# Performance work log

Measured on AMD Instinct MI355X. Metric: run time of the kernel, lower is better.

Reference implementation:

```python
import jax, jax.numpy as jnp
import numpy as np

B, S, HID, H = 8, 1024, 2048, 16
D = HID // H  # head dim 128
MAX_LEN, SCALE_BASE, THETA_BASE, EPS = 1024, 512.0, 10000.0, 1e-5


def setup_inputs() -> dict:
    key = jax.random.key(0)
    ks = jax.random.split(key, 10)
    std = 0.02
    n_layers_scale = std / np.sqrt(24.0)
    return {
        "activations": jax.random.normal(ks[0], (B, S, HID), jnp.float32),
        "cache_k": jnp.zeros((B, MAX_LEN, H, D), jnp.float32),
        "cache_v": jnp.zeros((B, MAX_LEN, H, D), jnp.float32),
        "index": 0,
        "ln1_w": jnp.ones((HID,), jnp.float32),
        "ln2_w": jnp.ones((HID,), jnp.float32),
        "q_w": std * jax.random.normal(ks[1], (HID, HID), jnp.float32),
        "k_w": std * jax.random.normal(ks[2], (HID, HID), jnp.float32),
        "v_w": std * jax.random.normal(ks[3], (HID, HID), jnp.float32),
        "o_w": n_layers_scale * jax.random.normal(ks[4], (HID, HID), jnp.float32),
        "w1": std * jax.random.normal(ks[5], (4 * HID, HID), jnp.float32),
        "w2": n_layers_scale * jax.random.normal(ks[6], (HID, 4 * HID), jnp.float32),
    }


def _ln(x, w):
    m = jnp.mean(x, axis=-1, keepdims=True)
    v = jnp.mean((x - m) ** 2, axis=-1, keepdims=True)
    return (x - m) * jax.lax.rsqrt(v + EPS) * w


def _rotate_every_two(x):
    return jnp.stack((-x[..., 1::2], x[..., 0::2]), axis=-1).reshape(x.shape)


def _xpos_consts(start, end):
    drange = jnp.arange(2, D + 2, 2, dtype=jnp.float32)
    theta = jnp.repeat((1.0 / THETA_BASE) ** (drange / D), 2)
    alpha = 0.4 * D
    zeta = jnp.repeat((drange / (D / 2) + alpha) / (1 + alpha), 2)
    half = MAX_LEN // 2
    seq = (jnp.arange(-half, MAX_LEN - half, dtype=jnp.float32) / SCALE_BASE)[start:end]
    seq = seq[:, None, None]  # [S,1,1]
    c = jnp.cos(seq * theta[None, None, :])  # [S,1,D]
    s = jnp.sin(seq * theta[None, None, :])
    t = zeta[None, None, :] ** seq
    return c, s, t


def reference(activations, cache_k, cache_v, index, ln1_w, ln2_w, q_w, k_w, v_w, o_w, w1, w2):
    xn = _ln(activations, ln1_w)
    q = (xn @ q_w.T).reshape(B, S, H, D)
    k = (xn @ k_w.T).reshape(B, S, H, D)
    v = (xn @ v_w.T).reshape(B, S, H, D)
    # NOTE: source applies xpos to (keys, values), exactly as written
    c, s, t = _xpos_consts(index, index + S)
    k = (k * c + _rotate_every_two(k) * s) * t
    v = (v * c + _rotate_every_two(v) * s) / t
    # index==0 and S==MAX_LEN -> get_full_kv returns incoming kv, mask None (causal)
    scale = 1.0 / np.sqrt(D)
    scores = jnp.einsum("bqhd,bkhd->bhqk", q, k) * scale
    causal = jnp.tril(jnp.ones((S, S), bool))
    scores = jnp.where(causal[None, None], scores, -jnp.inf)
    attn = jax.nn.softmax(scores, axis=-1)
    ctx = jnp.einsum("bhqk,bkhd->bqhd", attn, v).reshape(B, S, HID)
    acts = activations + ctx @ o_w.T
    h = jax.nn.gelu(_ln(acts, ln2_w) @ w1.T, approximate=False)
    acts = acts + h @ w2.T
    return acts, cache_k, cache_v
```

## Files before the change

### kernel.cpp

```cpp
#include <hip/hip_runtime.h>
#include <hip/hip_bf16.h>
#include <math.h>

#define B_ 8
#define S_ 1024
#define HID_ 2048
#define H_ 16
#define D_ 128

typedef __attribute__((ext_vector_type(8))) short bf16x8;
typedef __attribute__((ext_vector_type(4))) float f32x4;

__device__ inline unsigned short f2b_raw(float f){
  union { __hip_bfloat16 h; unsigned short u; } cv; cv.h = __float2bfloat16(f); return cv.u;
}

__device__ inline void async_copy16(const void* g, void* l){
  __builtin_amdgcn_global_load_lds((const __attribute__((address_space(1))) unsigned int*)g,
                                   (__attribute__((address_space(3))) unsigned int*)l, 16, 0, 0);
}

__global__ __launch_bounds__(256) void cvt_all(const float* __restrict__ qw, const float* __restrict__ kw,
                                               const float* __restrict__ vw, const float* __restrict__ ow,
                                               const float* __restrict__ w1, const float* __restrict__ w2,
                                               unsigned short* __restrict__ dst){
  int i = blockIdx.x*256 + threadIdx.x;
  if (i >= 12582912) return;
  const float* src;
  int local;
  if      (i <  1048576){ src = qw; local = i; }
  else if (i <  2097152){ src = kw; local = i - 1048576; }
  else if (i <  3145728){ src = vw; local = i - 2097152; }
  else if (i <  4194304){ src = ow; local = i - 3145728; }
  else if (i <  8388608){ src = w1; local = i - 4194304; }
  else                  { src = w2; local = i - 8388608; }
  float4 f = ((const float4*)src)[local];
  ushort4 o;
  o.x = f2b_raw(f.x); o.y = f2b_raw(f.y); o.z = f2b_raw(f.z); o.w = f2b_raw(f.w);
  ((ushort4*)dst)[i] = o;
}

__global__ __launch_bounds__(256) void ln_kernel(const float* __restrict__ x,
                                                 const float* __restrict__ w,
                                                 unsigned short* __restrict__ y){
  const int row = blockIdx.x, tid = threadIdx.x;
  const float* xr = x + (size_t)row*HID_;
  float4 a = ((const float4*)xr)[tid];
  float4 b = ((const float4*)xr)[tid+256];
  float s  = a.x+a.y+a.z+a.w + b.x+b.y+b.z+b.w;
  float ss = a.x*a.x+a.y*a.y+a.z*a.z+a.w*a.w + b.x*b.x+b.y*b.y+b.z*b.z+b.w*b.w;
  #pragma unroll
  for (int off=1; off<64; off<<=1){ s += __shfl_xor(s, off, 64); ss += __shfl_xor(ss, off, 64); }
  __shared__ float red[8];
  int wv = tid>>6;
  if ((tid&63)==0){ red[wv]=s; red[4+wv]=ss; }
  __syncthreads();
  s  = red[0]+red[1]+red[2]+red[3];
  ss = red[4]+red[5]+red[6]+red[7];
  float mean = s * (1.0f/HID_);
  float var  = ss * (1.0f/HID_) - mean*mean;
  float rstd = rsqrtf(var + 1e-5f);
  float4 w0 = ((const float4*)w)[tid];
  float4 w1v = ((const float4*)w)[tid+256];
  ushort4 o0, o1;
  o0.x = f2b_raw((a.x-mean)*rstd*w0.x); o0.y = f2b_raw((a.y-mean)*rstd*w0.y);
  o0.z = f2b_raw((a.z-mean)*rstd*w0.z); o0.w = f2b_raw((a.w-mean)*rstd*w0.w);
  o1.x = f2b_raw((b.x-mean)*rstd*w1v.x); o1.y = f2b_raw((b.y-mean)*rstd*w1v.y);
  o1.z = f2b_raw((b.z-mean)*rstd*w1v.z); o1.w = f2b_raw((b.w-mean)*rstd*w1v.w);
  *(ushort4*)(y + (size_t)row*HID_ + tid*4) = o0;
  *(ushort4*)(y + (size_t)row*HID_ + 1024 + tid*4) = o1;
}

template<int EPI, int TAG>
__global__ __launch_bounds__(256) void gemm_bt(
    const unsigned short* __restrict__ A, const unsigned short* __restrict__ W,
    unsigned short* __restrict__ out_b, float* __restrict__ out_f,
    const float* __restrict__ res,
    unsigned short* __restrict__ k_out, unsigned short* __restrict__ vt_out,
    const int* __restrict__ idxp,
    int M, int N, int K, float scale)
{
  __shared__ unsigned short smem[16384];
  unsigned short* sA = smem;
  unsigned short* sB = smem + 8192;
  const int tid = threadIdx.x;
  const int lane = tid & 63, wv = tid >> 6;
  const int wm = wv >> 1, wn = wv & 1;
  const int lm = lane & 15, lg = lane >> 4;
  const int m0 = blockIdx.y * 128, n0 = blockIdx.x * 128;

  f32x4 acc[4][4];
  #pragma unroll
  for (int r=0;r<4;r++)
    #pragma unroll
    for (int c=0;c<4;c++) acc[r][c] = (f32x4){0.f,0.f,0.f,0.f};

  int offA[4][2], offB[4][2];
  #pragma unroll
  for (int r=0;r<4;r++)
    #pragma unroll
    for (int kc=0;kc<2;kc++){
      int rowA = wm*64 + r*16 + lm;
      int rowB = wn*64 + r*16 + lm;
      offA[r][kc] = rowA*64 + (((kc*4+lg) ^ (lm&7))*8);
      offB[r][kc] = rowB*64 + (((kc*4+lg) ^ (lm&7))*8);
    }

  for (int kk=0; kk<K; kk+=64){
    #pragma unroll
    for (int i=0;i<4;i++){
      int unit = i*256 + tid;
      int row = unit >> 3, us = unit & 7;
      int ku = us ^ (row & 7);
      int ldsoff = (unit & ~63) * 8;
      async_copy16(A + (size_t)(m0+row)*K + kk + ku*8, sA + ldsoff);
      async_copy16(W + (size_t)(n0+row)*K + kk + ku*8, sB + ldsoff);
    }
    __syncthreads();
    #pragma unroll
    for (int kc=0;kc<2;kc++){
      bf16x8 af[4], bfr[4];
      #pragma unroll
      for (int r=0;r<4;r++) af[r]  = *(const bf16x8*)(sA + offA[r][kc]);
      #pragma unroll
      for (int c=0;c<4;c++) bfr[c] = *(const bf16x8*)(sB + offB[c][kc]);
      #pragma unroll
      for (int r=0;r<4;r++)
        #pragma unroll
        for (int c=0;c<4;c++)
          acc[r][c] = __builtin_amdgcn_mfma_f32_16x16x32_bf16(af[r], bfr[c], acc[r][c], 0,0,0);
    }
    __syncthreads();
  }

  if (EPI == 0){
    const int region = n0 >> 11;
    const int idx0 = idxp[0];
    const int b  = m0 >> 10;
    const int s0g = m0 & 1023;
    const int hh = (n0 & 2047) >> 7;
    #pragma unroll
    for (int r=0;r<4;r++){
      #pragma unroll
      for (int c=0;c<4;c++){
        const int row0 = m0 + wm*64 + r*16 + lg*4;
        const int col  = n0 + wn*64 + c*16 + lm;
        const int d = col & 127;
        const int s0 = row0 & 1023;
        if (region == 0){
          #pragma unroll
          for (int g=0; g<4; g++)
            out_b[(((size_t)b*H_ + hh)*S_ + s0 + g)*D_ + d] = f2b_raw(acc[r][c][g]*scale);
        } else {
          const float fp = (float)((d>>1) + 1);
          const float theta = exp2f(fp * -0.2076205059304601f);
          const float zeta  = (fp*0.03125f + 51.2f) * (1.0f/52.2f);
          const float lz = log2f(zeta);
          const float sgn = (d & 1) ? 1.0f : -1.0f;
          #pragma unroll
          for (int g=0; g<4; g++){
            float va = acc[r][c][g];
            float part = __shfl_xor(va, 1, 64);
            float seq = ((float)(idx0 + s0 + g) - 512.0f) * (1.0f/512.0f);
            float ang = seq * theta;
            float sn, cc;
            __sincosf(ang, &sn, &cc);
            float rot = va*cc + sgn*part*sn;
            if (region == 1){
              float t = exp2f(seq * lz);
              k_out[(((size_t)b*H_ + hh)*S_ + s0 + g)*D_ + d] = f2b_raw(rot * t);
            } else {
              float ti = exp2f(-seq * lz);
              int d_local = wn*64 + c*16 + lm;
              int s_local = wm*64 + r*16 + lg*4 + g;
              int s8 = s_local >> 3;
              smem[d_local*128 + ((s8 ^ (d_local & 7))*8) + (s_local & 7)] = f2b_raw(rot * ti);
            }
          }
        }
      }
    }
    if (region == 2){
      __syncthreads();
      #pragma unroll
      for (int i=0;i<8;i++){
        int f = i*256 + tid;
        int dl = f >> 4, u = f & 15;
        int us = u ^ (dl & 7);
        uint4 val = *(const uint4*)(smem + dl*128 + us*8);
        *(uint4*)(vt_out + ((size_t)((size_t)b*H_ + hh)*D_ + dl)*S_ + s0g + u*8) = val;
      }
    }
  } else {
    #pragma unroll
    for (int r=0;r<4;r++){
      #pragma unroll
      for (int c=0;c<4;c++){
        int row0 = m0 + wm*64 + r*16 + lg*4;
        int col  = n0 + wn*64 + c*16 + lm;
        #pragma unroll
        for (int g=0; g<4; g++){
          int rr = row0 + g;
          float vacc = acc[r][c][g];
          if (EPI == 1){
            size_t o = (size_t)rr*N + col;
            out_f[o] = vacc + res[o];
          } else {
            size_t o = (size_t)rr*N + col;
            out_b[o] = f2b_raw(0.5f*vacc*(1.0f + erff(vacc*0.70710678118654752f)));
          }
        }
      }
    }
  }
}

__global__ __launch_bounds__(256) void flash_attn(
    const unsigned short* __restrict__ Q, const unsigned short* __restrict__ Kx,
    const unsigned short* __restrict__ VT, unsigned short* __restrict__ ctx)
{
  __shared__ unsigned short sK[64*136];
  __shared__ unsigned short sVT[128*72];
  __shared__ unsigned short sP[4][16*72];
  const int tid = threadIdx.x, lane = tid & 63, wv = tid >> 6;
  const int lm = lane & 15, lg = lane >> 4;
  const int qt = blockIdx.x, bh = blockIdx.y;
  const size_t base = (size_t)bh * S_ * D_;
  const int qr = qt*64 + wv*16;

  bf16x8 aq[4];
  #pragma unroll
  for (int kc=0;kc<4;kc++)
    aq[kc] = *(const bf16x8*)(Q + base + (size_t)(qr + lm)*D_ + kc*32 + lg*8);

  f32x4 accO[8];
  #pragma unroll
  for (int n=0;n<8;n++) accO[n] = (f32x4){0.f,0.f,0.f,0.f};
  float mrow[4] = {-INFINITY,-INFINITY,-INFINITY,-INFINITY};
  float lrow[4] = {0.f,0.f,0.f,0.f};
  unsigned short* myP = &sP[wv][0];

  for (int kt=0; kt<=qt; ++kt){
    int k0 = kt*64;
    __syncthreads();
    #pragma unroll
    for (int i=0;i<4;i++){
      int chunk = i*256 + tid;
      int krow = chunk >> 4, c8 = chunk & 15;
      *(uint4*)(sK + krow*136 + c8*8) = *(const uint4*)(Kx + base + (size_t)(k0+krow)*D_ + c8*8);
      int dd = chunk >> 3, c4 = chunk & 7;
      *(uint4*)(sVT + dd*72 + c4*8) = *(const uint4*)(VT + base + (size_t)dd*S_ + k0 + c4*8);
    }
    __syncthreads();
    f32x4 sc[4];
    #pragma unroll
    for (int n=0;n<4;n++){
      sc[n] = (f32x4){0.f,0.f,0.f,0.f};
      #pragma unroll
      for (int kc=0;kc<4;kc++){
        bf16x8 bk = *(const bf16x8*)(sK + (n*16+lm)*136 + kc*32 + lg*8);
        sc[n] = __builtin_amdgcn_mfma_f32_16x16x32_bf16(aq[kc], bk, sc[n], 0,0,0);
      }
    }
    if (kt == qt){
      #pragma unroll
      for (int n=0;n<4;n++)
        #pragma unroll
        for (int g=0; g<4; g++)
          if (k0 + n*16 + lm > qr + lg*4 + g) sc[n][g] = -INFINITY;
    }
    float mnew[4], alpha[4];
    #pragma unroll
    for (int g=0; g<4; g++){
      float mx = fmaxf(fmaxf(sc[0][g], sc[1][g]), fmaxf(sc[2][g], sc[3][g]));
      #pragma unroll
      for (int off=1; off<16; off<<=1) mx = fmaxf(mx, __shfl_xor(mx, off, 16));
      mnew[g] = fmaxf(mrow[g], mx);
      alpha[g] = __expf(mrow[g] - mnew[g]);
      mrow[g] = mnew[g];
    }
    #pragma unroll
    for (int n=0;n<4;n++)
      #pragma unroll
      for (int g=0; g<4; g++)
        sc[n][g] = __expf(sc[n][g] - mnew[g]);
    #pragma unroll
    for (int g=0; g<4; g++){
      float sum = sc[0][g]+sc[1][g]+sc[2][g]+sc[3][g];
      #pragma unroll
      for (int off=1; off<16; off<<=1) sum += __shfl_xor(sum, off, 16);
      lrow[g] = lrow[g]*alpha[g] + sum;
    }
    #pragma unroll
    for (int n=0;n<8;n++)
      #pragma unroll
      for (int g=0; g<4; g++) accO[n][g] *= alpha[g];
    #pragma unroll
    for (int n=0;n<4;n++)
      #pragma unroll
      for (int g=0; g<4; g++)
        myP[(lg*4+g)*72 + n*16 + lm] = f2b_raw(sc[n][g]);
    #pragma unroll
    for (int kc=0;kc<2;kc++){
      bf16x8 ap = *(const bf16x8*)(myP + lm*72 + kc*32 + lg*8);
      #pragma unroll
      for (int n=0;n<8;n++){
        bf16x8 bv = *(const bf16x8*)(sVT + (n*16+lm)*72 + kc*32 + lg*8);
        accO[n] = __builtin_amdgcn_mfma_f32_16x16x32_bf16(ap, bv, accO[n], 0,0,0);
      }
    }
  }
  const int b = bh >> 4, hh = bh & 15;
  float rl[4];
  #pragma unroll
  for (int g=0; g<4; g++) rl[g] = 1.0f / lrow[g];
  #pragma unroll
  for (int n=0;n<8;n++)
    #pragma unroll
    for (int g=0; g<4; g++){
      int srow = qr + lg*4 + g;
      int d = n*16 + lm;
      ctx[(((size_t)b*S_ + srow)*H_ + hh)*D_ + d] = f2b_raw(accO[n][g]*rl[g]);
    }
}

extern "C" void kernel_launch(void* const* d_in, const int* in_sizes, int n_in,
                              void* d_out, int out_size, void* d_ws, size_t ws_size,
                              hipStream_t stream)
{
  (void)in_sizes; (void)n_in; (void)out_size; (void)ws_size;
  const float* acts   = (const float*)d_in[0];
  const float* cachek = (const float*)d_in[1];
  const float* cachev = (const float*)d_in[2];
  const int*   idxp   = (const int*)d_in[3];
  const float* ln1w   = (const float*)d_in[4];
  const float* ln2w   = (const float*)d_in[5];
  const float* qw     = (const float*)d_in[6];
  const float* kw     = (const float*)d_in[7];
  const float* vw     = (const float*)d_in[8];
  const float* ow     = (const float*)d_in[9];
  const float* w1     = (const float*)d_in[10];
  const float* w2     = (const float*)d_in[11];
  float* out = (float*)d_out;

  unsigned short* wqkv = (unsigned short*)d_ws;
  unsigned short* wo_b = wqkv + 12582912;
  unsigned short* w1_b = wo_b + 4194304;
  unsigned short* w2_b = w1_b + 16777216;
  unsigned short* xn   = w2_b + 16777216;
  unsigned short* qws  = xn   + 16777216;
  unsigned short* kws  = qws  + 16777216;
  unsigned short* vtws = kws  + 16777216;
  unsigned short* ctx  = vtws + 16777216;
  unsigned short* hbuf = qws;

  cvt_all<<<49152, 256, 0, stream>>>(qw, kw, vw, ow, w1, w2, wqkv);

  ln_kernel<<<8192, 256, 0, stream>>>(acts, ln1w, xn);

  gemm_bt<0,0><<<dim3(48,64), 256, 0, stream>>>(xn, wqkv, qws, nullptr, nullptr,
                                                kws, vtws, idxp,
                                                8192, 6144, 2048, 0.08838834764831845f);

  flash_attn<<<dim3(16,128), 256, 0, stream>>>(qws, kws, vtws, ctx);

  gemm_bt<1,1><<<dim3(16,64), 256, 0, stream>>>(ctx, wo_b, nullptr, out, acts,
                                                nullptr, nullptr, nullptr,
                                                8192, 2048, 2048, 1.0f);

  ln_kernel<<<8192, 256, 0, stream>>>(out, ln2w, xn);

  gemm_bt<2,2><<<dim3(64,64), 256, 0, stream>>>(xn, w1_b, hbuf, nullptr, nullptr,
                                                nullptr, nullptr, nullptr,
                                                8192, 8192, 2048, 1.0f);

  gemm_bt<1,3><<<dim3(16,64), 256, 0, stream>>>(hbuf, w2_b, nullptr, out, out,
                                                nullptr, nullptr, nullptr,
                                                8192, 2048, 8192, 1.0f);

  hipMemcpyAsync(out + 16777216, cachek, 67108864ull, hipMemcpyDeviceToDevice, stream);
  hipMemcpyAsync(out + 33554432, cachev, 67108864ull, hipMemcpyDeviceToDevice, stream);
}
```

Measured before the change: 1.807 ms.

## Rewrite GEMM as 256x256 tile with double-buffered LDS prefetch pipeline

Rebuilds the bf16 GEMM around 256x256 tiles, 512 threads and 8 waves, with a double-buffered 128KB LDS. The next K-slice is prefetched asynchronously in four chunks interleaved with MFMA phases, using explicit waitcnt/barrier and setprio. It also remaps workgroup IDs so neighbouring blocks share operands in L2. The aim is to raise MFMA utilisation and hide global latency, at the cost of high register and LDS pressure and fewer blocks per GEMM, which can hurt tail balance.

```diff
diff --git a/kernel.cpp b/kernel.cpp
--- a/kernel.cpp
+++ b/kernel.cpp
@@ -72,7 +72,7 @@
 }
 
 template<int EPI, int TAG>
-__global__ __launch_bounds__(256) void gemm_bt(
+__global__ __launch_bounds__(512, 2) void gemm_bt(
     const unsigned short* __restrict__ A, const unsigned short* __restrict__ W,
     unsigned short* __restrict__ out_b, float* __restrict__ out_f,
     const float* __restrict__ res,
@@ -80,57 +80,160 @@
     const int* __restrict__ idxp,
     int M, int N, int K, float scale)
 {
-  __shared__ unsigned short smem[16384];
-  unsigned short* sA = smem;
-  unsigned short* sB = smem + 8192;
+  (void)M;
+  __shared__ __align__(16) unsigned short smem[65536];
   const int tid = threadIdx.x;
   const int lane = tid & 63, wv = tid >> 6;
-  const int wm = wv >> 1, wn = wv & 1;
+  const int wm = wv >> 2, wn = wv & 3;
   const int lm = lane & 15, lg = lane >> 4;
-  const int m0 = blockIdx.y * 128, n0 = blockIdx.x * 128;
-
-  f32x4 acc[4][4];
-  #pragma unroll
-  for (int r=0;r<4;r++)
+
+  const int gx = gridDim.x;
+  const int nwg = gx * gridDim.y;
+  const int orig = blockIdx.y * gx + blockIdx.x;
+  const int wg = (orig & 7) * (nwg >> 3) + (orig >> 3);
+  const int bx = wg % gx, by = wg / gx;
+  const int m0 = by << 8, n0 = bx << 8;
+
+  f32x4 acc[8][4];
+  #pragma unroll
+  for (int r=0;r<8;r++)
     #pragma unroll
     for (int c=0;c<4;c++) acc[r][c] = (f32x4){0.f,0.f,0.f,0.f};
 
-  int offA[4][2], offB[4][2];
-  #pragma unroll
-  for (int r=0;r<4;r++)
-    #pragma unroll
-    for (int kc=0;kc<2;kc++){
-      int rowA = wm*64 + r*16 + lm;
-      int rowB = wn*64 + r*16 + lm;
-      offA[r][kc] = rowA*64 + (((kc*4+lg) ^ (lm&7))*8);
-      offB[r][kc] = rowB*64 + (((kc*4+lg) ^ (lm&7))*8);
-    }
-
-  for (int kk=0; kk<K; kk+=64){
-    #pragma unroll
-    for (int i=0;i<4;i++){
-      int unit = i*256 + tid;
-      int row = unit >> 3, us = unit & 7;
-      int ku = us ^ (row & 7);
-      int ldsoff = (unit & ~63) * 8;
-      async_copy16(A + (size_t)(m0+row)*K + kk + ku*8, sA + ldsoff);
-      async_copy16(W + (size_t)(n0+row)*K + kk + ku*8, sB + ldsoff);
-    }
-    __syncthreads();
-    #pragma unroll
-    for (int kc=0;kc<2;kc++){
-      bf16x8 af[4], bfr[4];
-      #pragma unroll
-      for (int r=0;r<4;r++) af[r]  = *(const bf16x8*)(sA + offA[r][kc]);
-      #pragma unroll
-      for (int c=0;c<4;c++) bfr[c] = *(const bf16x8*)(sB + offB[c][kc]);
-      #pragma unroll
-      for (int r=0;r<4;r++)
-        #pragma unroll
-        for (int c=0;c<4;c++)
-          acc[r][c] = __builtin_amdgcn_mfma_f32_16x16x32_bf16(af[r], bfr[c], acc[r][c], 0,0,0);
-    }
-    __syncthreads();
+  int oA[2], oB[2];
+  #pragma unroll
+  for (int kc=0;kc<2;kc++){
+    const int swz = ((kc*4+lg) ^ (lm&7)) * 8;
+    oA[kc] = wm*8192 + lm*64 + swz;
+    oB[kc] = wn*4096 + lm*64 + swz;
+  }
+
+  int sOffA[2][2], sLdsA[2][2], sOffB[2][2], sLdsB[2][2];
+  #pragma unroll
+  for (int j=0;j<2;j++){
+    const int unit = j*512 + tid;
+    const int r7 = unit >> 3, u = unit & 7;
+    const int r7g = (unit & ~63) >> 3;
+    #pragma unroll
+    for (int ch=0; ch<2; ch++){
+      const int rowA  = (r7  & 63) + ((r7  & 64) << 1) + ch*64;
+      const int rowA0 = (r7g & 63) + ((r7g & 64) << 1) + ch*64;
+      sOffA[ch][j] = rowA*K + (u ^ (rowA & 7))*8;
+      sLdsA[ch][j] = __builtin_amdgcn_readfirstlane(rowA0*64);
+      const int rowB  = (r7  & 31) + ((r7  & 96) << 1) + ch*32;
+      const int rowB0 = (r7g & 31) + ((r7g & 96) << 1) + ch*32;
+      sOffB[ch][j] = rowB*K + (u ^ (rowB & 7))*8;
+      sLdsB[ch][j] = __builtin_amdgcn_readfirstlane(rowB0*64);
+    }
+  }
+
+  const unsigned short* Ab = A + (size_t)m0 * K;
+  const unsigned short* Wb = W + (size_t)n0 * K;
+
+  #pragma unroll
+  for (int j=0;j<2;j++){
+    async_copy16(Ab + sOffA[0][j], smem + sLdsA[0][j]);
+    async_copy16(Ab + sOffA[1][j], smem + sLdsA[1][j]);
+    async_copy16(Wb + sOffB[0][j], smem + 16384 + sLdsB[0][j]);
+    async_copy16(Wb + sOffB[1][j], smem + 16384 + sLdsB[1][j]);
+  }
+  asm volatile("s_waitcnt vmcnt(0)\n\ts_barrier" ::: "memory");
+
+  const int T = K >> 6;
+  bf16x8 a[4][2], b[4][2];
+
+  for (int t=0; t<T; ++t){
+    const int cs = (t & 1) << 15;
+    const unsigned short* sAc = smem + cs;
+    const unsigned short* sBc = sAc + 16384;
+    unsigned short* dA = smem + (cs ^ 32768);
+    unsigned short* dB = dA + 16384;
+    const int kk = (t + 1) << 6;
+    const bool pf = (t + 1 < T);
+
+    #pragma unroll
+    for (int r=0;r<4;r++)
+      #pragma unroll
+      for (int kc=0;kc<2;kc++)
+        a[r][kc] = *(const bf16x8*)(sAc + oA[kc] + r*1024);
+    #pragma unroll
+    for (int c=0;c<2;c++)
+      #pragma unroll
+      for (int kc=0;kc<2;kc++)
+        b[c][kc] = *(const bf16x8*)(sBc + oB[kc] + c*1024);
+    if (pf){ async_copy16(Ab + sOffA[0][0] + kk, dA + sLdsA[0][0]);
+             async_copy16(Ab + sOffA[0][1] + kk, dA + sLdsA[0][1]);
+             asm volatile("s_waitcnt vmcnt(4)\n\ts_barrier" ::: "memory"); }
+    else   { asm volatile("s_waitcnt vmcnt(0)\n\ts_barrier" ::: "memory"); }
+    __builtin_amdgcn_sched_barrier(0);
+    __builtin_amdgcn_s_setprio(1);
+    #pragma unroll
+    for (int r=0;r<4;r++)
+      #pragma unroll
+      for (int c=0;c<2;c++)
+        #pragma unroll
+        for (int kc=0;kc<2;kc++)
+          acc[r][c] = __builtin_amdgcn_mfma_f32_16x16x32_bf16(a[r][kc], b[c][kc], acc[r][c], 0,0,0);
+    __builtin_amdgcn_s_setprio(0);
+    asm volatile("s_barrier" ::: "memory");
+
+    #pragma unroll
+    for (int c=0;c<2;c++)
+      #pragma unroll
+      for (int kc=0;kc<2;kc++)
+        b[2+c][kc] = *(const bf16x8*)(sBc + oB[kc] + (2+c)*1024);
+    if (pf){ async_copy16(Wb + sOffB[0][0] + kk, dB + sLdsB[0][0]);
+             async_copy16(Wb + sOffB[0][1] + kk, dB + sLdsB[0][1]);
+             asm volatile("s_waitcnt vmcnt(4)\n\ts_barrier" ::: "memory"); }
+    else   { asm volatile("s_waitcnt vmcnt(0)\n\ts_barrier" ::: "memory"); }
+    __builtin_amdgcn_sched_barrier(0);
+    __builtin_amdgcn_s_setprio(1);
+    #pragma unroll
+    for (int r=0;r<4;r++)
+      #pragma unroll
+      for (int c=0;c<2;c++)
+        #pragma unroll
+        for (int kc=0;kc<2;kc++)
+          acc[r][2+c] = __builtin_amdgcn_mfma_f32_16x16x32_bf16(a[r][kc], b[2+c][kc], acc[r][2+c], 0,0,0);
+    __builtin_amdgcn_s_setprio(0);
+    asm volatile("s_barrier" ::: "memory");
+
+    #pragma unroll
+    for (int r=0;r<4;r++)
+      #pragma unroll
+      for (int kc=0;kc<2;kc++)
+        a[r][kc] = *(const bf16x8*)(sAc + oA[kc] + 4096 + r*1024);
+    if (pf){ async_copy16(Wb + sOffB[1][0] + kk, dB + sLdsB[1][0]);
+             async_copy16(Wb + sOffB[1][1] + kk, dB + sLdsB[1][1]);
+             asm volatile("s_waitcnt vmcnt(4)\n\ts_barrier" ::: "memory"); }
+    else   { asm volatile("s_waitcnt vmcnt(0)\n\ts_barrier" ::: "memory"); }
+    __builtin_amdgcn_sched_barrier(0);
+    __builtin_amdgcn_s_setprio(1);
+    #pragma unroll
+    for (int r=0;r<4;r++)
+      #pragma unroll
+      for (int c=0;c<2;c++)
+        #pragma unroll
+        for (int kc=0;kc<2;kc++)
+          acc[4+r][2+c] = __builtin_amdgcn_mfma_f32_16x16x32_bf16(a[r][kc], b[2+c][kc], acc[4+r][2+c], 0,0,0);
+    __builtin_amdgcn_s_setprio(0);
+    asm volatile("s_barrier" ::: "memory");
+
+    if (pf){ async_copy16(Ab + sOffA[1][0] + kk, dA + sLdsA[1][0]);
+             async_copy16(Ab + sOffA[1][1] + kk, dA + sLdsA[1][1]);
+             asm volatile("s_waitcnt vmcnt(4)\n\ts_barrier" ::: "memory"); }
+    else   { asm volatile("s_waitcnt vmcnt(0)\n\ts_barrier" ::: "memory"); }
+    __builtin_amdgcn_sched_barrier(0);
+    __builtin_amdgcn_s_setprio(1);
+    #pragma unroll
+    for (int r=0;r<4;r++)
+      #pragma unroll
+      for (int c=0;c<2;c++)
+        #pragma unroll
+        for (int kc=0;kc<2;kc++)
+          acc[4+r][c] = __builtin_amdgcn_mfma_f32_16x16x32_bf16(a[r][kc], b[c][kc], acc[4+r][c], 0,0,0);
+    __builtin_amdgcn_s_setprio(0);
+    asm volatile("s_barrier" ::: "memory");
   }
 
   if (EPI == 0){
@@ -138,19 +241,18 @@
     const int idx0 = idxp[0];
     const int b  = m0 >> 10;
     const int s0g = m0 & 1023;
-    const int hh = (n0 & 2047) >> 7;
-    #pragma unroll
-    for (int r=0;r<4;r++){
+    const int hh = ((n0 & 2047) >> 7) + (wn >> 1);
+    const int db = (wn & 1) * 64;
+    #pragma unroll
+    for (int r=0;r<8;r++){
       #pragma unroll
       for (int c=0;c<4;c++){
-        const int row0 = m0 + wm*64 + r*16 + lg*4;
-        const int col  = n0 + wn*64 + c*16 + lm;
-        const int d = col & 127;
-        const int s0 = row0 & 1023;
+        const int srow = s0g + wm*128 + r*16 + lg*4;
+        const int d = db + c*16 + lm;
         if (region == 0){
           #pragma unroll
           for (int g=0; g<4; g++)
-            out_b[(((size_t)b*H_ + hh)*S_ + s0 + g)*D_ + d] = f2b_raw(acc[r][c][g]*scale);
+            out_b[(((size_t)b*H_ + hh)*S_ + srow + g)*D_ + d] = f2b_raw(acc[r][c][g]*scale);
         } else {
           const float fp = (float)((d>>1) + 1);
           const float theta = exp2f(fp * -0.2076205059304601f);
@@ -161,20 +263,20 @@
           for (int g=0; g<4; g++){
             float va = acc[r][c][g];
             float part = __shfl_xor(va, 1, 64);
-            float seq = ((float)(idx0 + s0 + g) - 512.0f) * (1.0f/512.0f);
+            float seq = ((float)(idx0 + srow + g) - 512.0f) * (1.0f/512.0f);
             float ang = seq * theta;
             float sn, cc;
             __sincosf(ang, &sn, &cc);
             float rot = va*cc + sgn*part*sn;
             if (region == 1){
-              float t = exp2f(seq * lz);
-              k_out[(((size_t)b*H_ + hh)*S_ + s0 + g)*D_ + d] = f2b_raw(rot * t);
+              float tt = exp2f(seq * lz);
+              k_out[(((size_t)b*H_ + hh)*S_ + srow + g)*D_ + d] = f2b_raw(rot * tt);
             } else {
               float ti = exp2f(-seq * lz);
               int d_local = wn*64 + c*16 + lm;
-              int s_local = wm*64 + r*16 + lg*4 + g;
+              int s_local = wm*128 + r*16 + lg*4 + g;
               int s8 = s_local >> 3;
-              smem[d_local*128 + ((s8 ^ (d_local & 7))*8) + (s_local & 7)] = f2b_raw(rot * ti);
+              smem[d_local*256 + ((s8 ^ (d_local & 7))*8) + (s_local & 7)] = f2b_raw(rot * ti);
             }
           }
         }
@@ -183,30 +285,29 @@
     if (region == 2){
       __syncthreads();
       #pragma unroll
-      for (int i=0;i<8;i++){
-        int f = i*256 + tid;
-        int dl = f >> 4, u = f & 15;
+      for (int i=0;i<16;i++){
+        int f = i*512 + tid;
+        int dl = f >> 5, u = f & 31;
         int us = u ^ (dl & 7);
-        uint4 val = *(const uint4*)(smem + dl*128 + us*8);
-        *(uint4*)(vt_out + ((size_t)((size_t)b*H_ + hh)*D_ + dl)*S_ + s0g + u*8) = val;
+        uint4 val = *(const uint4*)(smem + dl*256 + us*8);
+        int hh2 = ((n0 & 2047) >> 7) + (dl >> 7);
+        *(uint4*)(vt_out + ((size_t)((size_t)b*H_ + hh2)*D_ + (dl & 127))*S_ + s0g + u*8) = val;
       }
     }
   } else {
     #pragma unroll
-    for (int r=0;r<4;r++){
+    for (int r=0;r<8;r++){
       #pragma unroll
       for (int c=0;c<4;c++){
-        int row0 = m0 + wm*64 + r*16 + lg*4;
-        int col  = n0 + wn*64 + c*16 + lm;
+        const int row0 = m0 + wm*128 + r*16 + lg*4;
+        const int col  = n0 + wn*64 + c*16 + lm;
         #pragma unroll
         for (int g=0; g<4; g++){
-          int rr = row0 + g;
           float vacc = acc[r][c][g];
+          size_t o = (size_t)(row0 + g)*N + col;
           if (EPI == 1){
-            size_t o = (size_t)rr*N + col;
             out_f[o] = vacc + res[o];
           } else {
-            size_t o = (size_t)rr*N + col;
             out_b[o] = f2b_raw(0.5f*vacc*(1.0f + erff(vacc*0.70710678118654752f)));
           }
         }
@@ -358,25 +459,25 @@
 
   ln_kernel<<<8192, 256, 0, stream>>>(acts, ln1w, xn);
 
-  gemm_bt<0,0><<<dim3(48,64), 256, 0, stream>>>(xn, wqkv, qws, nullptr, nullptr,
+  gemm_bt<0,0><<<dim3(24,32), 512, 0, stream>>>(xn, wqkv, qws, nullptr, nullptr,
                                                 kws, vtws, idxp,
                                                 8192, 6144, 2048, 0.08838834764831845f);
 
   flash_attn<<<dim3(16,128), 256, 0, stream>>>(qws, kws, vtws, ctx);
 
-  gemm_bt<1,1><<<dim3(16,64), 256, 0, stream>>>(ctx, wo_b, nullptr, out, acts,
-                                                nullptr, nullptr, nullptr,
-                                                8192, 2048, 2048, 1.0f);
+  gemm_bt<1,1><<<dim3(8,32), 512, 0, stream>>>(ctx, wo_b, nullptr, out, acts,
+                                               nullptr, nullptr, nullptr,
+                                               8192, 2048, 2048, 1.0f);
 
   ln_kernel<<<8192, 256, 0, stream>>>(out, ln2w, xn);
 
-  gemm_bt<2,2><<<dim3(64,64), 256, 0, stream>>>(xn, w1_b, hbuf, nullptr, nullptr,
+  gemm_bt<2,2><<<dim3(32,32), 512, 0, stream>>>(xn, w1_b, hbuf, nullptr, nullptr,
                                                 nullptr, nullptr, nullptr,
                                                 8192, 8192, 2048, 1.0f);
 
-  gemm_bt<1,3><<<dim3(16,64), 256, 0, stream>>>(hbuf, w2_b, nullptr, out, out,
-                                                nullptr, nullptr, nullptr,
-                                                8192, 2048, 8192, 1.0f);
+  gemm_bt<1,3><<<dim3(8,32), 512, 0, stream>>>(hbuf, w2_b, nullptr, out, out,
+                                               nullptr, nullptr, nullptr,
+                                               8192, 2048, 8192, 1.0f);
 
   hipMemcpyAsync(out + 16777216, cachek, 67108864ull, hipMemcpyDeviceToDevice, stream);
   hipMemcpyAsync(out + 33554432, cachev, 67108864ull, hipMemcpyDeviceToDevice, stream);
```

After: 1.576 ms. -12.8%, faster.
